# Optimization experiments

Measured on AMD Instinct MI355X. Metric: run time of the kernel, lower is better.

## Reference

```python
import jax, jax.numpy as jnp
import numpy as np

V, E, U, D, B, T = 32000, 256, 512, 512, 32, 64


def setup_inputs() -> dict:
    key = jax.random.key(0)
    ks = jax.random.split(key, 12)
    g = lambda k, shape: (jax.random.normal(k, shape, jnp.float32) * 0.05)
    return dict(
        x=jax.random.randint(ks[0], (B, T), 0, V),
        emb=g(ks[1], (V, E)),
        Wxf=g(ks[2], (E, 4 * U)), Whf=g(ks[3], (U, 4 * U)), bf=jnp.zeros((4 * U,), jnp.float32),
        Wxb=g(ks[4], (E, 4 * U)), Whb=g(ks[5], (U, 4 * U)), bb=jnp.zeros((4 * U,), jnp.float32),
        W1=g(ks[6], (2 * U + D, 10)), b1=jnp.zeros((10,), jnp.float32),
        W2=g(ks[7], (10, 1)), b2=jnp.zeros((1,), jnp.float32),
        Wxd=g(ks[8], (2 * U, 4 * D)), Whd=g(ks[9], (D, 4 * D)), bd=jnp.zeros((4 * D,), jnp.float32),
        Wo=g(ks[10], (D, V)), bo=jnp.zeros((V,), jnp.float32),
    )


def lstm_cell(x_t, h, c, Wx, Wh, b):
    # Keras gate order: i, f, g(cell), o
    z = x_t @ Wx + h @ Wh + b
    i, f, g, o = jnp.split(z, 4, axis=-1)
    c = jax.nn.sigmoid(f) * c + jax.nn.sigmoid(i) * jnp.tanh(g)
    h = jax.nn.sigmoid(o) * jnp.tanh(c)
    return h, c


def lstm_seq(xs, Wx, Wh, b):
    # xs: [T, B, F] -> hidden states [T, B, units]
    units = Wh.shape[0]
    h0 = jnp.zeros((xs.shape[1], units), xs.dtype)

    def step(carry, x_t):
        h, c = lstm_cell(x_t, carry[0], carry[1], Wx, Wh, b)
        return (h, c), h

    _, hs = jax.lax.scan(step, (h0, h0), xs)
    return hs


def reference(x, emb, Wxf, Whf, bf, Wxb, Whb, bb, W1, b1, W2, b2, Wxd, Whd, bd, Wo, bo):
    Bsz, Tlen = x.shape
    xe = emb[x]                              # [B, T, E]
    xs = jnp.swapaxes(xe, 0, 1)              # [T, B, E]
    hf = lstm_seq(xs, Wxf, Whf, bf)          # forward direction
    hb = lstm_seq(xs[::-1], Wxb, Whb, bb)[::-1]  # backward direction
    a = jnp.swapaxes(jnp.concatenate([hf, hb], axis=-1), 0, 1)  # [B, T, 2U]
    du = Whd.shape[0]

    def dec_step(carry, _):
        h, c = carry
        s_rep = jnp.broadcast_to(h[:, None, :], (Bsz, Tlen, du))
        cat = jnp.concatenate([a, s_rep], axis=-1)              # [B, T, 2U+D]
        e = jax.nn.relu(jnp.tanh(cat @ W1 + b1) @ W2 + b2)      # [B, T, 1]
        score = jax.nn.softmax(e, axis=1)
        ctx = jnp.sum(score * a, axis=1)                        # [B, 2U]
        h, c = lstm_cell(ctx, h, c, Wxd, Whd, bd)
        out = jax.nn.softmax(h @ Wo + bo, axis=-1)              # [B, V]
        return (h, c), out

    init = (jnp.zeros((Bsz, du), a.dtype), jnp.zeros((Bsz, du), a.dtype))
    _, outs = jax.lax.scan(dec_step, init, None, length=Tlen)
    return jnp.swapaxes(outs, 0, 1)  # [B, T, V]
```

## Files before the change

### kernel.cpp

```cpp
#include <hip/hip_runtime.h>
#include <hip/hip_bf16.h>
#include <cstdint>

typedef float f32x4 __attribute__((ext_vector_type(4)));
typedef __bf16 bf16x8 __attribute__((ext_vector_type(8)));

__device__ __forceinline__ uint32_t bf1(float x) {
  uint32_t u = __float_as_uint(x);
  return (u + 0x7fffu + ((u >> 16) & 1u)) >> 16;
}
__device__ __forceinline__ uint32_t bpack(float lo, float hi) {
  return bf1(lo) | (bf1(hi) << 16);
}
__device__ __forceinline__ float blo(uint32_t u) { return __uint_as_float(u << 16); }
__device__ __forceinline__ float bhi(uint32_t u) { return __uint_as_float(u & 0xffff0000u); }
__device__ __forceinline__ float sigm(float x) {
  return __fdividef(1.f, 1.f + exp2f(x * -1.4426950408889634f));
}
__device__ __forceinline__ float tanhf_fast(float x) {
  float e2 = exp2f(x * 2.8853900817779268f);
  return 1.f - __fdividef(2.f, e2 + 1.f);
}

__device__ __forceinline__ float dot2bf(uint32_t a, uint32_t b, float acc) {
  asm("v_dot2_f32_bf16 %0, %1, %2, %0" : "+v"(acc) : "v"(a), "v"(b));
  return acc;
}

#define GLOAD_LDS16(g, l)                                                     \
  __builtin_amdgcn_global_load_lds(                                           \
      (const __attribute__((address_space(1))) void*)(g),                     \
      (__attribute__((address_space(3))) void*)(l), 16, 0, 0)

__global__ __launch_bounds__(256) void k0_pack(
    const float* __restrict__ Whf, const float* __restrict__ Whb,
    uint32_t* __restrict__ Wencp, const float* __restrict__ Whd,
    uint32_t* __restrict__ Wdp, const float* __restrict__ W1,
    uint32_t* __restrict__ W1pbAll)
{
  int bid = blockIdx.x;
  if (bid < 4096) {
    int p = bid * 256 + threadIdx.x;
    int e = p & 3, c = (p >> 2) & 7, k4p = (p >> 5) & 63;
    int blk = (p >> 11) & 255, dir = p >> 19;
    int k2 = 4 * k4p + e;
    const float* W = dir ? Whb : Whf;
    int col = (c >> 1) * 512 + blk * 2 + (c & 1);
    Wencp[p] = bpack(W[(size_t)(2 * k2) * 2048 + col],
                     W[(size_t)(2 * k2 + 1) * 2048 + col]);
  } else if (bid < 6144) {
    int p = (bid - 4096) * 256 + threadIdx.x;
    int e = p & 3, cc = (p >> 2) & 31, q4 = (p >> 7) & 63, ug = p >> 13;
    int k2 = 4 * q4 + e;
    int col = (cc >> 3) * 512 + ug * 8 + (cc & 7);
    int k = 2 * k2;
    Wdp[p] = bpack(Whd[(size_t)k * 2048 + col], Whd[(size_t)(k + 1) * 2048 + col]);
  } else {
    int p = (bid - 6144) * 256 + threadIdx.x;
    if (p < 9216) {
      int q = p / 12, j = p % 12;
      float v0 = (j < 10) ? W1[(size_t)(2 * q) * 10 + j] : 0.f;
      float v1 = (j < 10) ? W1[(size_t)(2 * q + 1) * 10 + j] : 0.f;
      W1pbAll[p] = bpack(v0, v1);
    }
  }
}

__global__ __launch_bounds__(256) void k1_embed_gemm(
    const int* __restrict__ x, const float* __restrict__ emb,
    const float* __restrict__ Wxf, const float* __restrict__ Wxb,
    const float* __restrict__ bfv, const float* __restrict__ bbv,
    float* __restrict__ Xf, float* __restrict__ Xb)
{
  __shared__ float As[32 * 260];
  __shared__ float Bs[32 * 128];
  __shared__ int xid[32];
  const int t = threadIdx.x;
  const int ty = blockIdx.y;
  const int c0 = blockIdx.x * 128;
  if (t < 32) xid[t] = x[t * 64 + ty];
  __syncthreads();
  for (int i = 0; i < 8; ++i) {
    int f4 = t + 256 * i;
    int r = f4 >> 6, k4 = (f4 & 63) << 2;
    float4 v = *(const float4*)(emb + (size_t)xid[r] * 256 + k4);
    *(float4*)(&As[r * 260 + k4]) = v;
  }
  const int isB = (c0 >= 2048);
  const float* Wsrc = isB ? Wxb : Wxf;
  const float* bias = isB ? bbv : bfv;
  const int cbase = c0 & 2047;
  float acc[4][4] = {};
  const int rq = t >> 5;
  const int cq = t & 31;
  for (int kc = 0; kc < 8; ++kc) {
    int k0 = kc * 32;
    __syncthreads();
    for (int i = 0; i < 4; ++i) {
      int f4 = t + 256 * i;
      int k = f4 >> 5, c4 = (f4 & 31) << 2;
      *(float4*)(&Bs[k * 128 + c4]) =
          *(const float4*)(Wsrc + (size_t)(k0 + k) * 2048 + cbase + c4);
    }
    __syncthreads();
#pragma unroll
    for (int kk = 0; kk < 32; ++kk) {
      float a0 = As[(4 * rq + 0) * 260 + k0 + kk];
      float a1 = As[(4 * rq + 1) * 260 + k0 + kk];
      float a2 = As[(4 * rq + 2) * 260 + k0 + kk];
      float a3 = As[(4 * rq + 3) * 260 + k0 + kk];
      float4 b = *(const float4*)(&Bs[kk * 128 + 4 * cq]);
      acc[0][0] += a0 * b.x; acc[0][1] += a0 * b.y; acc[0][2] += a0 * b.z; acc[0][3] += a0 * b.w;
      acc[1][0] += a1 * b.x; acc[1][1] += a1 * b.y; acc[1][2] += a1 * b.z; acc[1][3] += a1 * b.w;
      acc[2][0] += a2 * b.x; acc[2][1] += a2 * b.y; acc[2][2] += a2 * b.z; acc[2][3] += a2 * b.w;
      acc[3][0] += a3 * b.x; acc[3][1] += a3 * b.y; acc[3][2] += a3 * b.z; acc[3][3] += a3 * b.w;
    }
  }
  float* Xout = isB ? Xb : Xf;
  for (int i = 0; i < 4; ++i) {
    int c = cbase + 4 * cq + i;
    float bi = bias[c];
    for (int j = 0; j < 4; ++j) {
      int b_ = 4 * rq + j;
      Xout[((size_t)ty * 2048 + c) * 32 + b_] = acc[j][i] + bi;
    }
  }
}

__global__ __launch_bounds__(256) void k2_enc_step(
    const float* __restrict__ Xf, const float* __restrict__ Xb,
    const uint32_t* __restrict__ Wencp,
    const uint32_t* __restrict__ hfi, uint32_t* __restrict__ hfo,
    const uint32_t* __restrict__ hbi, uint32_t* __restrict__ hbo,
    float* __restrict__ cf, float* __restrict__ cb,
    ushort* __restrict__ aB, int step)
{
  __shared__ uint32_t hTp[256 * 32];
  __shared__ uint32_t Wsp[2048];
  __shared__ float zx[8 * 33];
  __shared__ float zbuf[32 * 9];
  __shared__ float hl[2 * 32];
  const int t = threadIdx.x;
  const int dir = blockIdx.x >> 8;
  const int blk = blockIdx.x & 255;
  const int u0 = blk * 2;
  const float* XF = dir ? Xb : Xf;
  const uint32_t* hin = dir ? hbi : hfi;
  uint32_t* hout = dir ? hbo : hfo;
  float* cst = dir ? cb : cf;
  const int ta = dir ? (63 - step) : step;
  const uint32_t* wsrc = Wencp + ((size_t)dir * 256 + blk) * 2048;

  for (int i = 0; i < 8; ++i) {
    int b4 = (t >> 6) * 64 + 256 * i;
    GLOAD_LDS16(hin + (size_t)(t + 256 * i) * 4, hTp + (size_t)b4 * 4);
  }
  for (int i = 0; i < 2; ++i) {
    int b4 = (t >> 6) * 64 + 256 * i;
    GLOAD_LDS16(wsrc + (size_t)(t + 256 * i) * 4, Wsp + (size_t)b4 * 4);
  }
  {
    int c = t >> 5, r = t & 31;
    int col = (c >> 1) * 512 + u0 + (c & 1);
    zx[c * 33 + r] = XF[((size_t)ta * 2048 + col) * 32 + r];
  }
  __syncthreads();
  const int r = t & 31, cc = t >> 5;
  float acc = zx[cc * 33 + r];
  const uint4* hT4 = (const uint4*)hTp;
  const uint4* Ws4 = (const uint4*)Wsp;
#pragma unroll 8
  for (int k4p = 0; k4p < 64; ++k4p) {
    uint4 ua = hT4[k4p * 32 + r];
    uint4 w = Ws4[k4p * 8 + cc];
    acc = dot2bf(ua.x, w.x, acc);
    acc = dot2bf(ua.y, w.y, acc);
    acc = dot2bf(ua.z, w.z, acc);
    acc = dot2bf(ua.w, w.w, acc);
  }
  zbuf[r * 9 + cc] = acc;
  __syncthreads();
  if (t < 64) {
    int rr = t & 31, j = t >> 5;
    float zi = zbuf[rr * 9 + j];
    float zf = zbuf[rr * 9 + 2 + j];
    float zg = zbuf[rr * 9 + 4 + j];
    float zo = zbuf[rr * 9 + 6 + j];
    int u = u0 + j;
    float cold = cst[u * 32 + rr];
    float cn = sigm(zf) * cold + sigm(zi) * tanhf_fast(zg);
    float h = sigm(zo) * tanhf_fast(cn);
    cst[u * 32 + rr] = cn;
    aB[((size_t)rr * 64 + ta) * 1024 + dir * 512 + u] = (ushort)bf1(h);
    hl[j * 32 + rr] = h;
  }
  __syncthreads();
  if (t < 32) {
    hout[(blk >> 2) * 128 + t * 4 + (blk & 3)] = bpack(hl[t], hl[32 + t]);
  }
}

__global__ __launch_bounds__(256) void k5_aw1(
    const ushort* __restrict__ aB, const uint32_t* __restrict__ W1pbAll,
    const float* __restrict__ b1, float* __restrict__ aw1)
{
  __shared__ uint32_t ar[512];
  __shared__ float ps[16 * 17];
  const int t = threadIdx.x;
  const uint32_t* aBu = (const uint32_t*)aB;
  for (int m = blockIdx.x; m < 2048; m += gridDim.x) {
    __syncthreads();
    *(uint2*)(&ar[t * 2]) = *(const uint2*)(aBu + (size_t)m * 512 + t * 2);
    __syncthreads();
    int j = t & 15, part = t >> 4;
    int jj = j < 10 ? j : 0;
    float s = 0.f;
#pragma unroll 8
    for (int q = part * 32; q < part * 32 + 32; ++q)
      s = dot2bf(ar[q], W1pbAll[q * 12 + jj], s);
    ps[part * 17 + j] = s;
    __syncthreads();
    if (t < 16) {
      float sum = 0.f;
      if (t < 10) {
        for (int p = 0; p < 16; ++p) sum += ps[p * 17 + t];
        sum += b1[t];
      }
      aw1[m * 16 + t] = sum;
    }
  }
}

__global__ __launch_bounds__(256) void k_wxdT(
    const float* __restrict__ Wxd, ushort* __restrict__ WxdT)
{
  __shared__ float tile[64 * 65];
  const int t = threadIdx.x;
  const int n0 = blockIdx.x * 64, k0 = blockIdx.y * 64;
  for (int i = 0; i < 16; ++i) {
    int p = t + 256 * i;
    int kk = p >> 6, nn = p & 63;
    tile[kk * 65 + nn] = Wxd[(size_t)(k0 + kk) * 2048 + n0 + nn];
  }
  __syncthreads();
  for (int i = 0; i < 4; ++i) {
    int p = t + 256 * i;
    int nn = p >> 4, k4 = (p & 15) * 4;
    ushort4 o;
    o.x = (ushort)bf1(tile[(k4 + 0) * 65 + nn]);
    o.y = (ushort)bf1(tile[(k4 + 1) * 65 + nn]);
    o.z = (ushort)bf1(tile[(k4 + 2) * 65 + nn]);
    o.w = (ushort)bf1(tile[(k4 + 3) * 65 + nn]);
    *(ushort4*)(WxdT + (size_t)(n0 + nn) * 1024 + k0 + k4) = o;
  }
}

__global__ __launch_bounds__(256) void kA_aprime(
    const ushort* __restrict__ WxdT, const ushort* __restrict__ aB,
    uint32_t* __restrict__ ApTb)
{
  __shared__ ushort As[128 * 64];
  __shared__ ushort Bs[128 * 64];
  const int t = threadIdx.x;
  const int lane = t & 63, w = t >> 6;
  const int wr = w >> 1, wc = w & 1;
  const int m0 = blockIdx.y * 128, n0 = blockIdx.x * 128;
  const int lrow = lane >> 3, s = lane & 7;
  const int quad = lane >> 4, l15 = lane & 15;
  f32x4 acc[4][4] = {};
  for (int kc = 0; kc < 16; ++kc) {
    const int k0 = kc * 64;
    __syncthreads();
    for (int i = 0; i < 4; ++i) {
      int row = w * 32 + i * 8 + lrow;
      int k8 = s ^ (row & 7);
      GLOAD_LDS16(WxdT + (size_t)(m0 + row) * 1024 + k0 + k8 * 8,
                  As + (w * 32 + i * 8) * 64);
      GLOAD_LDS16(aB + (size_t)(n0 + row) * 1024 + k0 + k8 * 8,
                  Bs + (w * 32 + i * 8) * 64);
    }
    __syncthreads();
#pragma unroll
    for (int ks = 0; ks < 2; ++ks) {
      bf16x8 af[4], bfr[4];
      int kq = ks * 4 + quad;
#pragma unroll
      for (int mi = 0; mi < 4; ++mi) {
        int row = wr * 64 + mi * 16 + l15;
        int slot = kq ^ (row & 7);
        af[mi] = *(const bf16x8*)(As + row * 64 + slot * 8);
      }
#pragma unroll
      for (int ni = 0; ni < 4; ++ni) {
        int row = wc * 64 + ni * 16 + l15;
        int slot = kq ^ (row & 7);
        bfr[ni] = *(const bf16x8*)(Bs + row * 64 + slot * 8);
      }
#pragma unroll
      for (int mi = 0; mi < 4; ++mi)
#pragma unroll
        for (int ni = 0; ni < 4; ++ni)
          acc[mi][ni] = __builtin_amdgcn_mfma_f32_16x16x32_bf16(
              af[mi], bfr[ni], acc[mi][ni], 0, 0, 0);
    }
  }
#pragma unroll
  for (int mi = 0; mi < 4; ++mi) {
    int mbase = m0 + wr * 64 + mi * 16 + quad * 4;
#pragma unroll
    for (int reg = 0; reg < 4; ++reg) {
      int m = mbase + reg;
#pragma unroll
      for (int ni = 0; ni < 4; ++ni) {
        int n = n0 + wc * 64 + ni * 16 + l15;
        float v = acc[mi][ni][reg];
        float v2 = __shfl_xor(v, 1);
        if (!(l15 & 1))
          ApTb[(size_t)m * 1024 + (n >> 1)] = bpack(v, v2);
      }
    }
  }
}

__global__ __launch_bounds__(256) void k4_dec_step(
    const uint32_t* __restrict__ ApTb, const float* __restrict__ aw1,
    const uint32_t* __restrict__ W1pb, const float* __restrict__ W2,
    const float* __restrict__ b2, const uint32_t* __restrict__ hdp_in,
    const uint32_t* __restrict__ Wdp, const float* __restrict__ bd,
    uint32_t* __restrict__ hdp_out, float* __restrict__ cd,
    ushort* __restrict__ HsB, int step)
{
  __shared__ uint32_t W1s[256 * 12];
  __shared__ uint32_t hdT[1024];
  __shared__ uint32_t Wsp[8192];
  __shared__ float ph[64 * 4 * 12];
  __shared__ float hw1[4 * 12];
  __shared__ float esc[4 * 65];
  __shared__ uint32_t escp[4 * 33];
  __shared__ float pm[4 * 9];
  __shared__ float mrow[4], srow[4];
  __shared__ float w2s[12];
  __shared__ float zp[2][128];
  __shared__ float zbuf[4 * 33];
  __shared__ float hl[32];
  const int t = threadIdx.x;
  const int ug = blockIdx.x >> 3;
  const int rg = blockIdx.x & 7;
  const int u0 = ug * 8, r0 = rg * 4;
  for (int i = 0; i < 3; ++i) {
    int b4 = (t >> 6) * 64 + 256 * i;
    GLOAD_LDS16(W1pb + (size_t)(t + 256 * i) * 4, W1s + (size_t)b4 * 4);
  }
  {
    int q4 = t >> 2, rl0 = t & 3;
    int b4 = (t >> 6) * 64;
    GLOAD_LDS16(hdp_in + (size_t)(q4 * 32 + r0 + rl0) * 4, hdT + (size_t)b4 * 4);
  }
  if (t < 12) w2s[t] = (t < 10) ? W2[t] : 0.f;
  __syncthreads();
  {
    const uint32_t* wsrc = Wdp + (size_t)ug * 8192;
    for (int i = 0; i < 8; ++i) {
      int b4 = (t >> 6) * 64 + 256 * i;
      GLOAD_LDS16(wsrc + (size_t)(t + 256 * i) * 4, Wsp + (size_t)b4 * 4);
    }
  }
  {
    const int rl = t & 3, kp = t >> 2;
    const uint4* hd4 = (const uint4*)hdT;
    float acc[10] = {};
    {
      uint4 u4 = hd4[kp * 4 + rl];
      const uint32_t* w0 = &W1s[(4 * kp) * 12];
      const uint32_t* w1 = &W1s[(4 * kp + 1) * 12];
      const uint32_t* w2p = &W1s[(4 * kp + 2) * 12];
      const uint32_t* w3 = &W1s[(4 * kp + 3) * 12];
#pragma unroll
      for (int j = 0; j < 10; ++j) {
        acc[j] = dot2bf(u4.x, w0[j], acc[j]);
        acc[j] = dot2bf(u4.y, w1[j], acc[j]);
        acc[j] = dot2bf(u4.z, w2p[j], acc[j]);
        acc[j] = dot2bf(u4.w, w3[j], acc[j]);
      }
    }
#pragma unroll
    for (int j = 0; j < 10; ++j) ph[(kp * 4 + rl) * 12 + j] = acc[j];
  }
  __syncthreads();
  if (t < 40) {
    int rl = t / 10, j = t % 10;
    float s = 0.f;
#pragma unroll
    for (int p = 0; p < 64; ++p) s += ph[(p * 4 + rl) * 12 + j];
    hw1[rl * 12 + j] = s;
  }
  __syncthreads();
  const float b2v = b2[0];
  {
    int rl = t >> 6, tt = t & 63;
    size_t m = (size_t)(r0 + rl) * 64 + tt;
    const float4* aw = (const float4*)(aw1 + m * 16);
    float4 q0 = aw[0], q1 = aw[1], q2 = aw[2];
    const float* hw = &hw1[rl * 12];
    float e = b2v;
    e += tanhf_fast(q0.x + hw[0]) * w2s[0];
    e += tanhf_fast(q0.y + hw[1]) * w2s[1];
    e += tanhf_fast(q0.z + hw[2]) * w2s[2];
    e += tanhf_fast(q0.w + hw[3]) * w2s[3];
    e += tanhf_fast(q1.x + hw[4]) * w2s[4];
    e += tanhf_fast(q1.y + hw[5]) * w2s[5];
    e += tanhf_fast(q1.z + hw[6]) * w2s[6];
    e += tanhf_fast(q1.w + hw[7]) * w2s[7];
    e += tanhf_fast(q2.x + hw[8]) * w2s[8];
    e += tanhf_fast(q2.y + hw[9]) * w2s[9];
    esc[rl * 65 + tt] = fmaxf(e, 0.f);
  }
  __syncthreads();
  if (t < 32) {
    int rl = t >> 3, part = t & 7;
    float m = -1e30f;
    for (int i = 0; i < 8; ++i) m = fmaxf(m, esc[rl * 65 + part * 8 + i]);
    pm[rl * 9 + part] = m;
  }
  __syncthreads();
  if (t < 4) {
    float m = pm[t * 9];
    for (int p = 1; p < 8; ++p) m = fmaxf(m, pm[t * 9 + p]);
    mrow[t] = m;
  }
  __syncthreads();
  if (t < 32) {
    int rl = t >> 3, part = t & 7;
    float m = mrow[rl];
    float s = 0.f;
    for (int i = 0; i < 8; ++i) s += __expf(esc[rl * 65 + part * 8 + i] - m);
    pm[rl * 9 + part] = s;
  }
  __syncthreads();
  if (t < 4) {
    float s = 0.f;
    for (int p = 0; p < 8; ++p) s += pm[t * 9 + p];
    srow[t] = __fdividef(1.f, s);
  }
  __syncthreads();
  if (t < 128) {
    int rl = t >> 5, q = t & 31;
    float m = mrow[rl], s = srow[rl];
    float v0 = __expf(esc[rl * 65 + 2 * q] - m) * s;
    float v1 = __expf(esc[rl * 65 + 2 * q + 1] - m) * s;
    escp[rl * 33 + q] = bpack(v0, v1);
  }
  __syncthreads();
  {
    const int out = t & 127;
    const int ccB = out >> 2, rl = out & 3;
    const int kh = t >> 7;
    const int colg = (ccB >> 3) * 512 + u0 + (ccB & 7);
    float acc = 0.f;
    {
      const uint4* hd4 = (const uint4*)hdT;
      const uint4* wd4 = (const uint4*)Wsp;
#pragma unroll 8
      for (int q4 = kh * 32; q4 < kh * 32 + 32; ++q4) {
        uint4 ua = hd4[q4 * 4 + rl];
        uint4 ub = wd4[q4 * 32 + ccB];
        acc = dot2bf(ua.x, ub.x, acc);
        acc = dot2bf(ua.y, ub.y, acc);
        acc = dot2bf(ua.z, ub.z, acc);
        acc = dot2bf(ua.w, ub.w, acc);
      }
    }
    {
      const uint32_t* ap = ApTb + (size_t)colg * 1024 + (r0 + rl) * 32;
      const uint32_t* ep = &escp[rl * 33];
#pragma unroll
      for (int i8 = kh * 4; i8 < kh * 4 + 4; ++i8) {
        uint4 v = *(const uint4*)(ap + i8 * 4);
        acc = dot2bf(v.x, ep[4 * i8 + 0], acc);
        acc = dot2bf(v.y, ep[4 * i8 + 1], acc);
        acc = dot2bf(v.z, ep[4 * i8 + 2], acc);
        acc = dot2bf(v.w, ep[4 * i8 + 3], acc);
      }
    }
    zp[kh][out] = acc;
  }
  __syncthreads();
  if (t < 128) {
    int ccB = t >> 2, rl = t & 3;
    int colg = (ccB >> 3) * 512 + u0 + (ccB & 7);
    zbuf[rl * 33 + ccB] = zp[0][t] + zp[1][t] + bd[colg];
  }
  __syncthreads();
  if (t < 32) {
    int j = t >> 2, rr = t & 3;
    int u = u0 + j, rgl = r0 + rr;
    float zi = zbuf[rr * 33 + j];
    float zf = zbuf[rr * 33 + 8 + j];
    float zg = zbuf[rr * 33 + 16 + j];
    float zo = zbuf[rr * 33 + 24 + j];
    float cold = cd[u * 32 + rgl];
    float cn = sigm(zf) * cold + sigm(zi) * tanhf_fast(zg);
    float h = sigm(zo) * tanhf_fast(cn);
    cd[u * 32 + rgl] = cn;
    HsB[(size_t)(step * 32 + rgl) * 512 + u] = (ushort)bf1(h);
    hl[j * 4 + rr] = h;
  }
  __syncthreads();
  if (t < 16) {
    int p = t >> 2, rr = t & 3;
    hdp_out[ug * 128 + (r0 + rr) * 4 + p] =
        bpack(hl[(2 * p) * 4 + rr], hl[(2 * p + 1) * 4 + rr]);
  }
}

__global__ __launch_bounds__(256) void k_woT(
    const float* __restrict__ Wo, ushort* __restrict__ WoT)
{
  __shared__ float tile[64 * 65];
  const int t = threadIdx.x;
  const int n0 = blockIdx.x * 64, k0 = blockIdx.y * 64;
  for (int i = 0; i < 16; ++i) {
    int p = t + 256 * i;
    int kk = p >> 6, nn = p & 63;
    tile[kk * 65 + nn] = Wo[(size_t)(k0 + kk) * 32000 + n0 + nn];
  }
  __syncthreads();
  for (int i = 0; i < 4; ++i) {
    int p = t + 256 * i;
    int nn = p >> 4, k4 = (p & 15) * 4;
    ushort4 o;
    o.x = (ushort)bf1(tile[(k4 + 0) * 65 + nn]);
    o.y = (ushort)bf1(tile[(k4 + 1) * 65 + nn]);
    o.z = (ushort)bf1(tile[(k4 + 2) * 65 + nn]);
    o.w = (ushort)bf1(tile[(k4 + 3) * 65 + nn]);
    *(ushort4*)(WoT + (size_t)(n0 + nn) * 512 + k0 + k4) = o;
  }
}

__global__ __launch_bounds__(256) void k6_logits_mfma(
    const ushort* __restrict__ HsB, const ushort* __restrict__ WoT,
    const float* __restrict__ bo, float* __restrict__ out,
    float2* __restrict__ pstats, int moff)
{
  __shared__ ushort As[128 * 64];
  __shared__ ushort Bs[128 * 64];
  const int t = threadIdx.x;
  const int lane = t & 63, w = t >> 6;
  const int wr = w >> 1, wc = w & 1;
  const int m0 = (blockIdx.y + moff) * 128, n0 = blockIdx.x * 128;
  const int lrow = lane >> 3, s = lane & 7;
  const int quad = lane >> 4, l15 = lane & 15;
  f32x4 acc[4][4] = {};
  for (int kc = 0; kc < 8; ++kc) {
    const int k0 = kc * 64;
    __syncthreads();
    for (int i = 0; i < 4; ++i) {
      int row = w * 32 + i * 8 + lrow;
      int k8 = s ^ (row & 7);
      GLOAD_LDS16(HsB + (size_t)(m0 + row) * 512 + k0 + k8 * 8,
                  As + (w * 32 + i * 8) * 64);
      GLOAD_LDS16(WoT + (size_t)(n0 + row) * 512 + k0 + k8 * 8,
                  Bs + (w * 32 + i * 8) * 64);
    }
    __syncthreads();
#pragma unroll
    for (int ks = 0; ks < 2; ++ks) {
      bf16x8 af[4], bfr[4];
      int kq = ks * 4 + quad;
#pragma unroll
      for (int mi = 0; mi < 4; ++mi) {
        int row = wr * 64 + mi * 16 + l15;
        int slot = kq ^ (row & 7);
        af[mi] = *(const bf16x8*)(As + row * 64 + slot * 8);
      }
#pragma unroll
      for (int ni = 0; ni < 4; ++ni) {
        int row = wc * 64 + ni * 16 + l15;
        int slot = kq ^ (row & 7);
        bfr[ni] = *(const bf16x8*)(Bs + row * 64 + slot * 8);
      }
#pragma unroll
      for (int mi = 0; mi < 4; ++mi)
#pragma unroll
        for (int ni = 0; ni < 4; ++ni)
          acc[mi][ni] = __builtin_amdgcn_mfma_f32_16x16x32_bf16(
              af[mi], bfr[ni], acc[mi][ni], 0, 0, 0);
    }
  }
  __syncthreads();
  float* pmx = (float*)As;
  float* psm = (float*)Bs;
#pragma unroll
  for (int mi = 0; mi < 4; ++mi) {
    int mbase = m0 + wr * 64 + mi * 16 + quad * 4;
#pragma unroll
    for (int reg = 0; reg < 4; ++reg) {
      int m = mbase + reg;
      int rowl = (m - m0);
      size_t rowbase = ((size_t)(m & 31) * 64 + (m >> 5)) * 32000;
      float vs[4];
      float mx = -1e30f;
#pragma unroll
      for (int ni = 0; ni < 4; ++ni) {
        int n = n0 + wc * 64 + ni * 16 + l15;
        float v = acc[mi][ni][reg] + bo[n];
        out[rowbase + n] = v;
        vs[ni] = v;
        mx = fmaxf(mx, v);
      }
      float sl = __expf(vs[0] - mx) + __expf(vs[1] - mx) +
                 __expf(vs[2] - mx) + __expf(vs[3] - mx);
      pmx[rowl * 32 + wc * 16 + l15] = mx;
      psm[rowl * 32 + wc * 16 + l15] = sl;
    }
  }
  __syncthreads();
  if (t < 128) {
    float m = pmx[t * 32], sacc = psm[t * 32];
    for (int i = 1; i < 32; ++i) {
      float m2 = pmx[t * 32 + i], s2 = psm[t * 32 + i];
      float mn = fmaxf(m, m2);
      sacc = sacc * __expf(m - mn) + s2 * __expf(m2 - mn);
      m = mn;
    }
    int mg = m0 + t;
    int outrow = (mg & 31) * 64 + (mg >> 5);
    pstats[(size_t)outrow * 256 + blockIdx.x] = make_float2(m, sacc);
  }
}

__global__ __launch_bounds__(256) void k7_softmax(
    float* __restrict__ out, const float2* __restrict__ pstats, int half)
{
  __shared__ float mred[256], sred[256];
  const int t = threadIdx.x;
  const int mg = half * 1024 + blockIdx.x;
  const int row = (mg & 31) * 64 + (mg >> 5);
  float m = -1e30f, s = 0.f;
  if (t < 250) {
    float2 p = pstats[(size_t)row * 256 + t];
    m = p.x;
    s = p.y;
  }
  mred[t] = m;
  sred[t] = s;
  __syncthreads();
  for (int st = 128; st > 0; st >>= 1) {
    if (t < st) {
      float m1 = mred[t], m2 = mred[t + st];
      float mn = fmaxf(m1, m2);
      sred[t] = sred[t] * __expf(m1 - mn) + sred[t + st] * __expf(m2 - mn);
      mred[t] = mn;
    }
    __syncthreads();
  }
  m = mred[0];
  const float inv = 1.f / sred[0];
  float* p = out + (size_t)row * 32000;
  for (int i = t; i < 8000; i += 256) {
    float4 v = *(const float4*)(p + i * 4);
    v.x = __expf(v.x - m) * inv;
    v.y = __expf(v.y - m) * inv;
    v.z = __expf(v.z - m) * inv;
    v.w = __expf(v.w - m) * inv;
    *(float4*)(p + i * 4) = v;
  }
}

extern "C" void kernel_launch(void* const* d_in, const int* in_sizes, int n_in,
                              void* d_out, int out_size, void* d_ws, size_t ws_size,
                              hipStream_t stream)
{
  const int* x = (const int*)d_in[0];
  const float* emb = (const float*)d_in[1];
  const float* Wxf = (const float*)d_in[2];
  const float* Whf = (const float*)d_in[3];
  const float* bfv = (const float*)d_in[4];
  const float* Wxb = (const float*)d_in[5];
  const float* Whb = (const float*)d_in[6];
  const float* bbv = (const float*)d_in[7];
  const float* W1 = (const float*)d_in[8];
  const float* b1 = (const float*)d_in[9];
  const float* W2 = (const float*)d_in[10];
  const float* b2 = (const float*)d_in[11];
  const float* Wxd = (const float*)d_in[12];
  const float* Whd = (const float*)d_in[13];
  const float* bd = (const float*)d_in[14];
  const float* Wo = (const float*)d_in[15];
  const float* bo = (const float*)d_in[16];

  float* ws = (float*)d_ws;
  float* c_f = ws + 0;
  float* c_b = ws + 16384;
  float* c_d = ws + 32768;
  uint32_t* hfp0 = (uint32_t*)(ws + 49152);
  uint32_t* hfp1 = hfp0 + 8192;
  uint32_t* hbp0 = (uint32_t*)(ws + 65536);
  uint32_t* hbp1 = hbp0 + 8192;
  uint32_t* hdp0 = (uint32_t*)(ws + 81920);
  uint32_t* hdp1 = hdp0 + 8192;
  uint32_t* W1pbAll = (uint32_t*)(ws + 98304);
  uint32_t* Wencp = (uint32_t*)(ws + 114688);
  uint32_t* Wdp = (uint32_t*)(ws + 1163264);
  ushort* aB = (ushort*)(ws + 1687552);
  float* aw1 = ws + 2742272;
  float* Xf = ws + 2775040;
  float* Xb = Xf + 4194304;
  ushort* HsB = (ushort*)(ws + 13260800);
  uint32_t* ApTb = (uint32_t*)Xf;
  ushort* WxdT = (ushort*)Xb;
  ushort* WoT = (ushort*)Xf;
  float2* pstats = (float2*)Wencp;

  hipMemsetAsync(ws, 0, 98304 * sizeof(float), stream);

  k0_pack<<<6180, 256, 0, stream>>>(Whf, Whb, Wencp, Whd, Wdp, W1, W1pbAll);

  k1_embed_gemm<<<dim3(32, 64), 256, 0, stream>>>(x, emb, Wxf, Wxb, bfv, bbv, Xf, Xb);

  for (int s = 0; s < 64; ++s) {
    const uint32_t* hfi = (s & 1) ? hfp1 : hfp0;
    uint32_t* hfo = (s & 1) ? hfp0 : hfp1;
    const uint32_t* hbi = (s & 1) ? hbp1 : hbp0;
    uint32_t* hbo = (s & 1) ? hbp0 : hbp1;
    k2_enc_step<<<512, 256, 0, stream>>>(Xf, Xb, Wencp, hfi, hfo, hbi, hbo,
                                         c_f, c_b, aB, s);
  }

  k5_aw1<<<256, 256, 0, stream>>>(aB, W1pbAll, b1, aw1);
  k_wxdT<<<dim3(32, 16), 256, 0, stream>>>(Wxd, WxdT);
  kA_aprime<<<dim3(16, 16), 256, 0, stream>>>(WxdT, aB, ApTb);

  for (int s = 0; s < 64; ++s) {
    const uint32_t* hdi = (s & 1) ? hdp1 : hdp0;
    uint32_t* hdo = (s & 1) ? hdp0 : hdp1;
    k4_dec_step<<<512, 256, 0, stream>>>(ApTb, aw1, W1pbAll + 6144, W2, b2,
                                         hdi, Wdp, bd, hdo, c_d, HsB, s);
  }

  k_woT<<<dim3(500, 8), 256, 0, stream>>>(Wo, WoT);
  k6_logits_mfma<<<dim3(250, 8), 256, 0, stream>>>(HsB, WoT, bo,
                                                   (float*)d_out, pstats, 0);
  k7_softmax<<<1024, 256, 0, stream>>>((float*)d_out, pstats, 0);
  k6_logits_mfma<<<dim3(250, 8), 256, 0, stream>>>(HsB, WoT, bo,
                                                   (float*)d_out, pstats, 8);
  k7_softmax<<<1024, 256, 0, stream>>>((float*)d_out, pstats, 1);
}
```

Baseline: 1.612 ms.

## Use MFMA bf16 for encoder recurrent step with swizzled weight/hidden layout

Replaces the v_dot2-based per-thread dot products in the encoder LSTM step with 16x16x32 bf16 MFMA instructions. Each block now handles 16 batch rows by 4 units (16 gate columns) rather than all 32 rows by 2 units. The packed recurrent weights and the hidden-state output use a new XOR-swizzled row-major layout so the LDS reads avoid bank conflicts. Partial sums from the four waves are reduced through LDS, which adds a sync. The hidden-state format written by this kernel must match what other kernels read; any consumer elsewhere that reads hout in the old layout would break.

Result: faster. 1.527 ms (-5.2%).

```diff
diff --git a/kernel.cpp b/kernel.cpp
--- a/kernel.cpp
+++ b/kernel.cpp
@@ -41,13 +41,13 @@
   int bid = blockIdx.x;
   if (bid < 4096) {
     int p = bid * 256 + threadIdx.x;
-    int e = p & 3, c = (p >> 2) & 7, k4p = (p >> 5) & 63;
-    int blk = (p >> 11) & 255, dir = p >> 19;
-    int k2 = 4 * k4p + e;
+    int j2 = p & 3, slot = (p >> 2) & 63, c = (p >> 8) & 15;
+    int cg = (p >> 12) & 127, dir = p >> 19;
+    int k = slot * 8 + j2 * 2;
     const float* W = dir ? Whb : Whf;
-    int col = (c >> 1) * 512 + blk * 2 + (c & 1);
-    Wencp[p] = bpack(W[(size_t)(2 * k2) * 2048 + col],
-                     W[(size_t)(2 * k2 + 1) * 2048 + col]);
+    int colg = (c >> 2) * 512 + cg * 4 + (c & 3);
+    Wencp[p ^ ((c & 7) << 2)] =
+        bpack(W[(size_t)k * 2048 + colg], W[(size_t)(k + 1) * 2048 + colg]);
   } else if (bid < 6144) {
     int p = (bid - 4096) * 256 + threadIdx.x;
     int e = p & 3, cc = (p >> 2) & 31, q4 = (p >> 7) & 63, ug = p >> 13;
@@ -135,68 +135,79 @@
     float* __restrict__ cf, float* __restrict__ cb,
     ushort* __restrict__ aB, int step)
 {
-  __shared__ uint32_t hTp[256 * 32];
-  __shared__ uint32_t Wsp[2048];
-  __shared__ float zx[8 * 33];
-  __shared__ float zbuf[32 * 9];
-  __shared__ float hl[2 * 32];
+  __shared__ ushort Hs[16 * 512];
+  __shared__ ushort Ws[16 * 512];
+  __shared__ float zp[4 * 256];
+  __shared__ float zx[256];
+  __shared__ float zbuf[256];
+  __shared__ float hl[64];
   const int t = threadIdx.x;
   const int dir = blockIdx.x >> 8;
-  const int blk = blockIdx.x & 255;
-  const int u0 = blk * 2;
+  const int rh = (blockIdx.x >> 7) & 1;
+  const int cg = blockIdx.x & 127;
+  const int r0 = rh * 16, u0 = cg * 4;
   const float* XF = dir ? Xb : Xf;
   const uint32_t* hin = dir ? hbi : hfi;
   uint32_t* hout = dir ? hbo : hfo;
   float* cst = dir ? cb : cf;
   const int ta = dir ? (63 - step) : step;
-  const uint32_t* wsrc = Wencp + ((size_t)dir * 256 + blk) * 2048;
-
-  for (int i = 0; i < 8; ++i) {
-    int b4 = (t >> 6) * 64 + 256 * i;
-    GLOAD_LDS16(hin + (size_t)(t + 256 * i) * 4, hTp + (size_t)b4 * 4);
-  }
-  for (int i = 0; i < 2; ++i) {
-    int b4 = (t >> 6) * 64 + 256 * i;
-    GLOAD_LDS16(wsrc + (size_t)(t + 256 * i) * 4, Wsp + (size_t)b4 * 4);
-  }
+
   {
-    int c = t >> 5, r = t & 31;
-    int col = (c >> 1) * 512 + u0 + (c & 1);
-    zx[c * 33 + r] = XF[((size_t)ta * 2048 + col) * 32 + r];
-  }
-  __syncthreads();
-  const int r = t & 31, cc = t >> 5;
-  float acc = zx[cc * 33 + r];
-  const uint4* hT4 = (const uint4*)hTp;
-  const uint4* Ws4 = (const uint4*)Wsp;
-#pragma unroll 8
-  for (int k4p = 0; k4p < 64; ++k4p) {
-    uint4 ua = hT4[k4p * 32 + r];
-    uint4 w = Ws4[k4p * 8 + cc];
-    acc = dot2bf(ua.x, w.x, acc);
-    acc = dot2bf(ua.y, w.y, acc);
-    acc = dot2bf(ua.z, w.z, acc);
-    acc = dot2bf(ua.w, w.w, acc);
-  }
-  zbuf[r * 9 + cc] = acc;
+    const uint32_t* hinu = hin + r0 * 256;
+    for (int i = 0; i < 4; ++i) {
+      int b4 = (t >> 6) * 64 + 256 * i;
+      GLOAD_LDS16(hinu + (size_t)(t + 256 * i) * 4, (uint32_t*)Hs + b4 * 4);
+    }
+    const uint32_t* wsrc = Wencp + ((size_t)dir * 128 + cg) * 4096;
+    for (int i = 0; i < 4; ++i) {
+      int b4 = (t >> 6) * 64 + 256 * i;
+      GLOAD_LDS16(wsrc + (size_t)(t + 256 * i) * 4, (uint32_t*)Ws + b4 * 4);
+    }
+  }
+  {
+    int cl = t & 15, rl = t >> 4;
+    int colg = (cl >> 2) * 512 + u0 + (cl & 3);
+    zx[t] = XF[((size_t)ta * 2048 + colg) * 32 + r0 + rl];
+  }
+  __syncthreads();
+  const int lane = t & 63, w = t >> 6;
+  const int quad = lane >> 4, l15 = lane & 15;
+  f32x4 acc = {};
+#pragma unroll
+  for (int mm = 0; mm < 4; ++mm) {
+    int m = w * 4 + mm;
+    int slot = m * 4 + quad;
+    bf16x8 a = *(const bf16x8*)(Hs + l15 * 512 + (slot ^ (l15 & 7)) * 8);
+    bf16x8 b = *(const bf16x8*)(Ws + l15 * 512 + (slot ^ (l15 & 7)) * 8);
+    acc = __builtin_amdgcn_mfma_f32_16x16x32_bf16(a, b, acc, 0, 0, 0);
+  }
+#pragma unroll
+  for (int reg = 0; reg < 4; ++reg)
+    zp[w * 256 + (quad * 4 + reg) * 16 + l15] = acc[reg];
+  __syncthreads();
+  zbuf[t] = zp[t] + zp[256 + t] + zp[512 + t] + zp[768 + t] + zx[t];
   __syncthreads();
   if (t < 64) {
-    int rr = t & 31, j = t >> 5;
-    float zi = zbuf[rr * 9 + j];
-    float zf = zbuf[rr * 9 + 2 + j];
-    float zg = zbuf[rr * 9 + 4 + j];
-    float zo = zbuf[rr * 9 + 6 + j];
-    int u = u0 + j;
-    float cold = cst[u * 32 + rr];
+    int rl = t & 15, ui = t >> 4;
+    int u = u0 + ui, r = r0 + rl;
+    float zi = zbuf[rl * 16 + ui];
+    float zf = zbuf[rl * 16 + 4 + ui];
+    float zg = zbuf[rl * 16 + 8 + ui];
+    float zo = zbuf[rl * 16 + 12 + ui];
+    float cold = cst[u * 32 + r];
     float cn = sigm(zf) * cold + sigm(zi) * tanhf_fast(zg);
     float h = sigm(zo) * tanhf_fast(cn);
-    cst[u * 32 + rr] = cn;
-    aB[((size_t)rr * 64 + ta) * 1024 + dir * 512 + u] = (ushort)bf1(h);
-    hl[j * 32 + rr] = h;
-  }
-  __syncthreads();
-  if (t < 32) {
-    hout[(blk >> 2) * 128 + t * 4 + (blk & 3)] = bpack(hl[t], hl[32 + t]);
+    cst[u * 32 + r] = cn;
+    aB[((size_t)r * 64 + ta) * 1024 + dir * 512 + u] = (ushort)bf1(h);
+    hl[rl * 4 + ui] = h;
+  }
+  __syncthreads();
+  if (t < 16) {
+    int r = r0 + t;
+    uint32_t lo = bpack(hl[t * 4 + 0], hl[t * 4 + 1]);
+    uint32_t hi = bpack(hl[t * 4 + 2], hl[t * 4 + 3]);
+    uint32_t* dst = hout + r * 256 + (((cg >> 1) ^ (r & 7)) * 4) + (cg & 1) * 2;
+    *(uint2*)dst = make_uint2(lo, hi);
   }
 }
 
```
